# Performance work log

Hardware: AMD Instinct MI355X
Metric: run time of the kernel (lower is better)

Reference implementation:

```python
import jax, jax.numpy as jnp
import numpy as np

# Static dims (see shape_source)
B, S, D = 4, 4096, 1024      # batch, seq, d_model
H, E, K = 4096, 8, 2         # ffn hidden, num experts, top_k
GS = 128                     # group size = sqrt(B*S)
G = (B * S) // GS            # 128 groups, zero padding
CAP = 32                     # expert capacity after clamping


def setup_inputs() -> dict:
    key = jax.random.key(0)
    ks = jax.random.split(key, 8)
    std = jnp.float32(0.02)
    return {
        "x": jax.random.normal(ks[0], (B, S, D), jnp.float32),
        "gate_w": jax.random.normal(ks[1], (D, E), jnp.float32) * std,
        "gate_b": jnp.zeros((E,), jnp.float32),
        "keys": jax.random.normal(ks[2], (D, E, H), jnp.float32) * std,
        "key_b": jnp.zeros((E, H), jnp.float32),
        "values": jax.random.normal(ks[3], (H, E, D), jnp.float32) * std,
        "value_b": jnp.zeros((E, D), jnp.float32),
        "s_keys": jax.random.normal(ks[4], (D, 1, H), jnp.float32) * std,
        "s_key_b": jnp.zeros((1, H), jnp.float32),
        "s_values": jax.random.normal(ks[5], (H, 1, D), jnp.float32) * std,
        "s_value_b": jnp.zeros((1, D), jnp.float32),
    }


def reference(x, gate_w, gate_b, keys, key_b, values, value_b,
              s_keys, s_key_b, s_values, s_value_b):
    # ---- group tokens: [B,S,D] -> [G,GS,D] (B*S divisible by GS, no pad) ----
    xg = x.reshape(G, GS, D)

    # ---- Router (inference path: no aux loss) ----
    logits = jnp.einsum('gsd,de->gse', xg, gate_w) + gate_b          # [G,GS,E]
    probs = jax.nn.softmax(logits, axis=-1)
    gate, idx = jax.lax.top_k(probs, K)                              # [G,GS,K]
    mask = jax.nn.one_hot(idx, E, dtype=gate.dtype)                  # [G,GS,K,E]
    # position within each expert's capacity buffer (1-based where assigned)
    pos = jnp.cumsum(mask, axis=1) * mask                            # [G,GS,K,E]
    valid = (pos < CAP).astype(gate.dtype)
    pos_oh = jax.nn.one_hot(pos.astype(jnp.int32), CAP, dtype=gate.dtype)  # [G,GS,K,E,CAP]
    # combine tensor: sum over top-k, drop slot 0 (unassigned) -> [G,GS,E,CAP-1]
    combine = jnp.einsum('gsk,gske,gskec->gsec', gate, valid, pos_oh)[..., 1:]
    dispatch = (combine > 0).astype(x.dtype)                         # dispatch mask

    # ---- dispatch -> per-expert FFN -> combine ----
    exp_in = jnp.einsum('gsec,gsd->gecd', dispatch, xg)              # [G,E,CAP-1,D]
    h = jax.nn.gelu(jnp.einsum('gecd,deh->gech', exp_in, keys)
                    + key_b[None, :, None, :])                       # [G,E,CAP-1,H]
    eo = jnp.einsum('gech,hed->gecd', h, values) + value_b[None, :, None, :]
    moe = jnp.einsum('gsec,gecd->gsd', combine, eo)                  # [G,GS,D]

    # ---- shared expert (num_shared_experts == 1; mean over 1 is identity) ----
    sh = jax.nn.gelu(jnp.einsum('gsd,dh->gsh', xg, s_keys[:, 0, :]) + s_key_b[0])
    shared = jnp.einsum('gsh,hd->gsd', sh, s_values[:, 0, :]) + s_value_b[0]

    return (moe + shared).reshape(B, S, D)
```

## Files before the change

### kernel.cpp

```cpp
#include <hip/hip_runtime.h>
#include <hip/hip_bf16.h>

typedef unsigned short u16;
typedef __attribute__((ext_vector_type(8))) __bf16 bf16x8;
typedef __attribute__((ext_vector_type(4))) float f32x4;

#define TOK 16384
#define DM  1024
#define HD  4096
#define NE  8
#define NG  128
#define GSZ 128
#define CAPM 31
#define MEP (NG*32)

static __device__ __forceinline__ u16 f2b(float f) {
  union { float f; unsigned u; } v; v.f = f;
  unsigned r = v.u + 0x7fffu + ((v.u >> 16) & 1u);
  return (u16)(r >> 16);
}
static __device__ __forceinline__ float b2f(u16 u) {
  union { unsigned u; float f; } v; v.u = (unsigned)u << 16; return v.f;
}

static __device__ __forceinline__ float gelu_f(float x) {
  float y = 0.7978845608028654f * (x + 0.044715f * x * x * x);
  float t = __expf(-2.0f * fabsf(y));
  float th = (1.0f - t) / (1.0f + t);
  th = (y < 0.0f) ? -th : th;
  return 0.5f * x * (1.0f + th);
}

static __device__ __forceinline__ void gl2lds16(const void* g, void* l) {
  __builtin_amdgcn_global_load_lds(
      (const __attribute__((address_space(1))) void*)g,
      (__attribute__((address_space(3))) void*)l, 16, 0, 0);
}

__global__ __launch_bounds__(256) void k_router(
    const float* __restrict__ x, const float* __restrict__ gw,
    const float* __restrict__ gb, int* __restrict__ e_sel,
    float* __restrict__ gsel) {
  int wave = threadIdx.x >> 6, lane = threadIdx.x & 63;
  int t = blockIdx.x * 4 + wave;
  const float* xr = x + (size_t)t * DM;
  double acc[8] = {0,0,0,0,0,0,0,0};
  for (int d0 = lane * 4; d0 < DM; d0 += 256) {
    float4 xv = *(const float4*)(xr + d0);
    float xa[4] = {xv.x, xv.y, xv.z, xv.w};
    const float* g0 = gw + (size_t)d0 * NE;
#pragma unroll
    for (int dd = 0; dd < 4; ++dd)
#pragma unroll
      for (int e = 0; e < 8; ++e)
        acc[e] += (double)xa[dd] * (double)g0[dd * 8 + e];
  }
#pragma unroll
  for (int off = 32; off > 0; off >>= 1)
#pragma unroll
    for (int e = 0; e < 8; ++e)
      acc[e] += __shfl_down(acc[e], off, 64);
  if (lane == 0) {
    float l[8];
#pragma unroll
    for (int e = 0; e < 8; ++e) l[e] = (float)acc[e] + gb[e];
    int e0 = 0;
    for (int e = 1; e < 8; ++e) if (l[e] > l[e0]) e0 = e;
    int e1 = (e0 == 0) ? 1 : 0;
    for (int e = 0; e < 8; ++e) if (e != e0 && l[e] > l[e1]) e1 = e;
    float m = l[e0], s = 0.f, p[8];
    for (int e = 0; e < 8; ++e) { p[e] = expf(l[e] - m); s += p[e]; }
    e_sel[t] = e0; e_sel[TOK + t] = e1;
    gsel[t] = p[e0] / s; gsel[TOK + t] = p[e1] / s;
  }
}

__global__ void k_assign(const int* __restrict__ e_sel,
                         int* __restrict__ tok_slot, int* __restrict__ slot_tok) {
  int g = blockIdx.x;
  for (int i = threadIdx.x; i < NE * 32 * 2; i += 64) {
    int e = i >> 6, rem = i & 63, c = rem >> 1, k = rem & 1;
    slot_tok[((size_t)(e * MEP + g * 32 + c)) * 2 + k] = -1;
  }
  __syncthreads();
  if (threadIdx.x == 0) {
    int cnt[2][NE];
    for (int k = 0; k < 2; ++k) for (int e = 0; e < NE; ++e) cnt[k][e] = 0;
    for (int s = 0; s < GSZ; ++s) {
      int t = g * GSZ + s;
      for (int k = 0; k < 2; ++k) {
        int e = e_sel[k * TOK + t];
        int r = ++cnt[k][e];
        if (r <= CAPM) {
          int m = e * MEP + g * 32 + (r - 1);
          tok_slot[k * TOK + t] = m;
          slot_tok[(size_t)m * 2 + k] = t;
        } else tok_slot[k * TOK + t] = -1;
      }
    }
  }
}

__global__ __launch_bounds__(128) void k_build_expin(
    const float* __restrict__ x, const int* __restrict__ slot_tok,
    u16* __restrict__ exp_in) {
  int m = blockIdx.x;
  int t0 = slot_tok[(size_t)m * 2], t1 = slot_tok[(size_t)m * 2 + 1];
  int d = threadIdx.x * 8;
  float v[8] = {0,0,0,0,0,0,0,0};
  if (t0 >= 0) {
    const float4* p = (const float4*)(x + (size_t)t0 * DM + d);
    float4 a = p[0], b = p[1];
    v[0]+=a.x; v[1]+=a.y; v[2]+=a.z; v[3]+=a.w;
    v[4]+=b.x; v[5]+=b.y; v[6]+=b.z; v[7]+=b.w;
  }
  if (t1 >= 0) {
    const float4* p = (const float4*)(x + (size_t)t1 * DM + d);
    float4 a = p[0], b = p[1];
    v[0]+=a.x; v[1]+=a.y; v[2]+=a.z; v[3]+=a.w;
    v[4]+=b.x; v[5]+=b.y; v[6]+=b.z; v[7]+=b.w;
  }
  ushort4 o0, o1;
  o0.x=f2b(v[0]); o0.y=f2b(v[1]); o0.z=f2b(v[2]); o0.w=f2b(v[3]);
  o1.x=f2b(v[4]); o1.y=f2b(v[5]); o1.z=f2b(v[6]); o1.w=f2b(v[7]);
  *(ushort4*)(exp_in + (size_t)m * DM + d) = o0;
  *(ushort4*)(exp_in + (size_t)m * DM + d + 4) = o1;
}

__global__ __launch_bounds__(256) void k_cast_bf16(
    const float* __restrict__ in, u16* __restrict__ out, size_t n) {
  size_t i = ((size_t)blockIdx.x * 256 + threadIdx.x) * 4;
  if (i >= n) return;
  float4 v = *(const float4*)(in + i);
  ushort4 o; o.x=f2b(v.x); o.y=f2b(v.y); o.z=f2b(v.z); o.w=f2b(v.w);
  *(ushort4*)(out + i) = o;
}

__global__ __launch_bounds__(256) void k_transpose(
    const float* __restrict__ in, u16* __restrict__ out,
    int K, int N, int rs) {
  __shared__ float tile[32][33];
  int k0 = blockIdx.x * 32, n0 = blockIdx.y * 32;
  int tx = threadIdx.x & 31, ty = threadIdx.x >> 5;
#pragma unroll
  for (int i = 0; i < 4; ++i)
    tile[ty + i * 8][tx] = in[(size_t)(k0 + ty + i * 8) * rs + n0 + tx];
  __syncthreads();
#pragma unroll
  for (int i = 0; i < 4; ++i) {
    int n = ty + i * 8;
    out[(size_t)(n0 + n) * K + k0 + tx] = f2b(tile[tx][n]);
  }
}


#define PH_MID() \
  __builtin_amdgcn_s_barrier(); \
  __builtin_amdgcn_s_setprio(1);

#define PH_END() \
  __builtin_amdgcn_s_setprio(0); \
  asm volatile("s_waitcnt vmcnt(4)" ::: "memory"); \
  __builtin_amdgcn_s_barrier();

#define PH_END0() \
  __builtin_amdgcn_s_setprio(0); \
  asm volatile("s_waitcnt vmcnt(0)" ::: "memory"); \
  __builtin_amdgcn_s_barrier();

#define PH_ENDN() \
  __builtin_amdgcn_s_setprio(0); \
  __builtin_amdgcn_s_barrier();

#define STG(gp, ld, lds) \
  gl2lds16((gp) + (size_t)srow * (ld) + scol, (lds) + sdst); \
  gl2lds16((gp) + (size_t)(srow + 64) * (ld) + scol, (lds) + 4096 + sdst);

#define RD_A(SLOT) \
  _Pragma("unroll") for (int k2 = 0; k2 < 2; ++k2) \
    _Pragma("unroll") for (int mi = 0; mi < 4; ++mi) \
      a[k2][mi] = *(const bf16x8*)(&HA[SLOT][0] + offA[k2][mi]);

#define RD_BA(SLOT) \
  _Pragma("unroll") for (int k2 = 0; k2 < 2; ++k2) \
    _Pragma("unroll") for (int ni = 0; ni < 2; ++ni) \
      bA[k2][ni] = *(const bf16x8*)(&HB[SLOT][0] + offB[k2][ni]);

#define RD_BB(SLOT) \
  _Pragma("unroll") for (int k2 = 0; k2 < 2; ++k2) \
    _Pragma("unroll") for (int ni = 0; ni < 2; ++ni) \
      bB[k2][ni] = *(const bf16x8*)(&HB[SLOT][0] + offB[k2][ni]);

#define MM(BM, MOFF, NOFF) \
  _Pragma("unroll") for (int k2 = 0; k2 < 2; ++k2) \
    _Pragma("unroll") for (int mi = 0; mi < 4; ++mi) \
      _Pragma("unroll") for (int ni = 0; ni < 2; ++ni) \
        acc[mi + MOFF][ni + NOFF] = __builtin_amdgcn_mfma_f32_16x16x32_bf16( \
            a[k2][mi], BM[k2][ni], acc[mi + MOFF][ni + NOFF], 0, 0, 0);

#define TILE(T, SA0, SA1, SB0, SB1, DA0, DA1, DB0, DB1) { \
  const u16* An = Ab + ((T) + 1) * 64; \
  const u16* Bn = Bb + ((T) + 1) * 64; \
  RD_A(SA0); RD_BA(SB0); \
  STG(An, lda, &HA[DA0][0]); \
  PH_MID(); MM(bA, 0, 0); PH_END(); \
  RD_BB(SB1); \
  STG(Bn, ldb, &HB[DB0][0]); \
  PH_MID(); MM(bB, 0, 2); PH_END(); \
  RD_A(SA1); \
  STG(Bn + (size_t)128 * ldb, ldb, &HB[DB1][0]); \
  PH_MID(); MM(bB, 4, 2); PH_END(); \
  STG(An + (size_t)128 * lda, lda, &HA[DA1][0]); \
  PH_MID(); MM(bA, 4, 0); PH_END(); \
}

#define TILE_LAST(SA0, SA1, SB0, SB1) { \
  RD_A(SA0); RD_BA(SB0); \
  PH_MID(); MM(bA, 0, 0); PH_END0(); \
  RD_BB(SB1); \
  PH_MID(); MM(bB, 0, 2); PH_ENDN(); \
  RD_A(SA1); \
  PH_MID(); MM(bB, 4, 2); PH_ENDN(); \
  PH_MID(); MM(bA, 4, 0); PH_ENDN(); \
}

template <int EPI>
__global__ __launch_bounds__(512, 2) void k_gemm8p(
    const u16* __restrict__ A, size_t sAe, int lda,
    const u16* __restrict__ B, size_t sBe, int ldb,
    void* __restrict__ Cv, size_t sCe, int ldc,
    const float* __restrict__ bias, int sBiasE, int K, int gx, int gy) {
  __shared__ __align__(16) u16 HA[4][128 * 64];
  __shared__ __align__(16) u16 HB[4][128 * 64];
  const int tid = threadIdx.x;
  const int lane = tid & 63, wid = tid >> 6;
  const int wr = wid >> 2, wc = wid & 3;
  const int la15 = lane & 15, hi = lane >> 4;

  int nwg = gridDim.x, per = nwg >> 3;
  int wg = (blockIdx.x & 7) * per + (blockIdx.x >> 3);
  int bx = wg % gx, tmp = wg / gx;
  int by = tmp % gy, z = tmp / gy;

  const u16* Ab = A + (size_t)z * sAe + (size_t)(bx * 256) * lda;
  const u16* Bb = B + (size_t)z * sBe + (size_t)(by * 256) * ldb;

  int offA[2][4], offB[2][2];
#pragma unroll
  for (int k2 = 0; k2 < 2; ++k2) {
    int sl = k2 * 4 + hi;
#pragma unroll
    for (int mi = 0; mi < 4; ++mi) {
      int r = (mi * 2 + wr) * 16 + la15;
      offA[k2][mi] = r * 64 + ((sl ^ (r & 7)) << 3);
    }
#pragma unroll
    for (int ni = 0; ni < 2; ++ni) {
      int r = (ni * 4 + wc) * 16 + la15;
      offB[k2][ni] = r * 64 + ((sl ^ (r & 7)) << 3);
    }
  }
  const int srow = tid >> 3;
  const int scol = (((tid & 7) ^ (srow & 7)) << 3);
  const int sdst = (tid & ~63) * 8;

  f32x4 acc[8][4] = {};
  const int NT = K >> 6;

  bf16x8 a[2][4], bA[2][2], bB[2][2];

  STG(Ab, lda, &HA[0][0]);
  STG(Bb, ldb, &HB[0][0]);
  STG(Bb + (size_t)128 * ldb, ldb, &HB[1][0]);
  STG(Ab + (size_t)128 * lda, lda, &HA[1][0]);
  asm volatile("s_waitcnt vmcnt(0)" ::: "memory");
  __builtin_amdgcn_s_barrier();

  for (int t = 0; t + 2 < NT; t += 2) {
    TILE(t,     0, 1, 0, 1, 2, 3, 2, 3);
    TILE(t + 1, 2, 3, 2, 3, 0, 1, 0, 1);
  }
  TILE(NT - 2, 0, 1, 0, 1, 2, 3, 2, 3);
  TILE_LAST(2, 3, 2, 3);

  const int hi4 = hi << 2;
#pragma unroll
  for (int ni = 0; ni < 4; ++ni) {
    int col = by * 256 + (ni * 4 + wc) * 16 + la15;
    float bv = bias[(size_t)z * sBiasE + col];
#pragma unroll
    for (int mi = 0; mi < 8; ++mi) {
      int row0 = bx * 256 + (mi * 2 + wr) * 16 + hi4;
      f32x4 v = acc[mi][ni];
#pragma unroll
      for (int j = 0; j < 4; ++j) {
        int row = row0 + j;
        float val = v[j] + bv;
        if (EPI == 0)
          ((u16*)Cv)[(size_t)z * sCe + (size_t)row * ldc + col] = f2b(gelu_f(val));
        else if (EPI == 1)
          ((u16*)Cv)[(size_t)z * sCe + (size_t)row * ldc + col] = f2b(val);
        else
          ((float*)Cv)[(size_t)z * sCe + (size_t)row * ldc + col] = val;
      }
    }
  }
}

__global__ __launch_bounds__(256) void k_combine(
    const int* __restrict__ tok_slot, const float* __restrict__ gsel,
    const u16* __restrict__ eo, float* __restrict__ out) {
  int t = blockIdx.x;
  int d = threadIdx.x * 4;
  float4 v = *(float4*)(out + (size_t)t * DM + d);
#pragma unroll
  for (int k = 0; k < 2; ++k) {
    int m = tok_slot[k * TOK + t];
    if (m >= 0) {
      float g = gsel[k * TOK + t];
      ushort4 e = *(const ushort4*)(eo + (size_t)m * DM + d);
      v.x += g * b2f(e.x); v.y += g * b2f(e.y);
      v.z += g * b2f(e.z); v.w += g * b2f(e.w);
    }
  }
  *(float4*)(out + (size_t)t * DM + d) = v;
}

__global__ void k_report(float* out, float code) { out[0] = code; }

extern "C" void kernel_launch(void* const* d_in, const int* in_sizes, int n_in,
                              void* d_out, int out_size, void* d_ws, size_t ws_size,
                              hipStream_t stream) {
  (void)in_sizes; (void)n_in;
  const float* x     = (const float*)d_in[0];
  const float* gw    = (const float*)d_in[1];
  const float* gb    = (const float*)d_in[2];
  const float* keys  = (const float*)d_in[3];
  const float* keyb  = (const float*)d_in[4];
  const float* vals  = (const float*)d_in[5];
  const float* valb  = (const float*)d_in[6];
  const float* skey  = (const float*)d_in[7];
  const float* skeyb = (const float*)d_in[8];
  const float* sval  = (const float*)d_in[9];
  const float* svalb = (const float*)d_in[10];
  float* out = (float*)d_out;

  char* ws = (char*)d_ws;
  size_t off = 0;
  auto alloc = [&](size_t bytes) -> char* {
    char* p = ws + off; off += (bytes + 255) & ~(size_t)255; return p;
  };
  int*   e_sel    = (int*)  alloc(2 * TOK * 4);
  float* gsel     = (float*)alloc(2 * TOK * 4);
  int*   tok_slot = (int*)  alloc(2 * TOK * 4);
  int*   slot_tok = (int*)  alloc((size_t)NE * MEP * 2 * 4);

  size_t off_r1 = off;
  u16* xb     = (u16*)alloc((size_t)TOK * DM * 2);
  u16* skT    = (u16*)alloc((size_t)HD * DM * 2);
  u16* svT    = (u16*)alloc((size_t)DM * HD * 2);
  u16* exp_in = (u16*)alloc((size_t)NE * MEP * DM * 2);
  u16* eo = (u16*)(ws + off_r1);
  size_t eo_end = off_r1 + (size_t)NE * MEP * DM * 2;
  if (eo_end > off) off = eo_end;

  u16* keysT = (u16*)alloc((size_t)NE * HD * DM * 2);
  u16* valsT = (u16*)alloc((size_t)NE * DM * HD * 2);

  size_t sh_b = (size_t)TOK * HD * 2;
  size_t h_b  = (size_t)NE * MEP * HD * 2;
  u16* sh = (u16*)(ws + off);
  u16* h  = (u16*)(ws + off);
  size_t need = off + (sh_b > h_b ? sh_b : h_b);

  if (need > ws_size) {
    hipMemsetAsync(d_out, 0, (size_t)out_size * 4, stream);
    k_report<<<1, 1, 0, stream>>>(out, -(float)(ws_size >> 20));
    return;
  }

  k_router<<<TOK / 4, 256, 0, stream>>>(x, gw, gb, e_sel, gsel);
  k_assign<<<NG, 64, 0, stream>>>(e_sel, tok_slot, slot_tok);
  k_build_expin<<<NE * MEP, 128, 0, stream>>>(x, slot_tok, exp_in);

  k_cast_bf16<<<(TOK * DM / 4) / 256, 256, 0, stream>>>(x, xb, (size_t)TOK * DM);
  k_transpose<<<dim3(DM / 32, HD / 32), 256, 0, stream>>>(skey, skT, DM, HD, HD);
  k_transpose<<<dim3(HD / 32, DM / 32), 256, 0, stream>>>(sval, svT, HD, DM, DM);
  for (int e = 0; e < NE; ++e) {
    k_transpose<<<dim3(DM / 32, HD / 32), 256, 0, stream>>>(
        keys + (size_t)e * HD, keysT + (size_t)e * HD * DM, DM, HD, NE * HD);
    k_transpose<<<dim3(HD / 32, DM / 32), 256, 0, stream>>>(
        vals + (size_t)e * DM, valsT + (size_t)e * DM * HD, HD, DM, NE * DM);
  }

  k_gemm8p<0><<<(TOK/256)*(HD/256), 512, 0, stream>>>(
      xb, 0, DM, skT, 0, DM, sh, 0, HD, skeyb, 0, DM, TOK/256, HD/256);
  k_gemm8p<2><<<(TOK/256)*(DM/256), 512, 0, stream>>>(
      sh, 0, HD, svT, 0, HD, out, 0, DM, svalb, 0, HD, TOK/256, DM/256);

  k_gemm8p<0><<<(MEP/256)*(HD/256)*NE, 512, 0, stream>>>(
      exp_in, (size_t)MEP * DM, DM, keysT, (size_t)HD * DM, DM,
      h, (size_t)MEP * HD, HD, keyb, HD, DM, MEP/256, HD/256);
  k_gemm8p<1><<<(MEP/256)*(DM/256)*NE, 512, 0, stream>>>(
      h, (size_t)MEP * HD, HD, valsT, (size_t)DM * HD, HD,
      eo, (size_t)MEP * DM, DM, valb, DM, HD, MEP/256, DM/256);

  k_combine<<<TOK, 256, 0, stream>>>(tok_slot, gsel, eo, out);
}
```

Before: 1.244 ms.

## Software-pipeline LDS fragment reads with double-buffered A registers in GEMM

Restructures the GEMM main loop so that LDS fragment reads for the next phase are issued before the current phase's MFMAs. It adds a second A register buffer (aC/aN) and prefetches the next tile's A and B fragments at the end of each tile. The barriers drop from two per phase to one, with looser vmcnt waits, and the per-lane LDS offsets are simplified to base plus constant strides. The aim is to hide LDS latency behind MFMA work and cut synchronisation cost, at the price of higher register pressure under launch_bounds(512,2) and tighter reasoning about LDS hazards.

```diff
diff --git a/kernel.cpp b/kernel.cpp
--- a/kernel.cpp
+++ b/kernel.cpp
@@ -154,74 +154,62 @@
 }
 
 
-#define PH_MID() \
-  __builtin_amdgcn_s_barrier(); \
-  __builtin_amdgcn_s_setprio(1);
-
-#define PH_END() \
-  __builtin_amdgcn_s_setprio(0); \
-  asm volatile("s_waitcnt vmcnt(4)" ::: "memory"); \
-  __builtin_amdgcn_s_barrier();
-
-#define PH_END0() \
-  __builtin_amdgcn_s_setprio(0); \
-  asm volatile("s_waitcnt vmcnt(0)" ::: "memory"); \
-  __builtin_amdgcn_s_barrier();
-
-#define PH_ENDN() \
-  __builtin_amdgcn_s_setprio(0); \
-  __builtin_amdgcn_s_barrier();
+#define SP1() __builtin_amdgcn_s_setprio(1);
+#define SP0() __builtin_amdgcn_s_setprio(0);
+#define BAR() __builtin_amdgcn_s_barrier();
+#define VM2() asm volatile("s_waitcnt vmcnt(2)" ::: "memory");
+#define VM0() asm volatile("s_waitcnt vmcnt(0)" ::: "memory");
 
 #define STG(gp, ld, lds) \
   gl2lds16((gp) + (size_t)srow * (ld) + scol, (lds) + sdst); \
   gl2lds16((gp) + (size_t)(srow + 64) * (ld) + scol, (lds) + 4096 + sdst);
 
-#define RD_A(SLOT) \
+#define RD_A(DST, SLOT) \
   _Pragma("unroll") for (int k2 = 0; k2 < 2; ++k2) \
     _Pragma("unroll") for (int mi = 0; mi < 4; ++mi) \
-      a[k2][mi] = *(const bf16x8*)(&HA[SLOT][0] + offA[k2][mi]);
-
-#define RD_BA(SLOT) \
+      DST[k2][mi] = *(const bf16x8*)(&HA[SLOT][0] + offAk[k2] + mi * 2048);
+
+#define RD_B(DST, SLOT) \
   _Pragma("unroll") for (int k2 = 0; k2 < 2; ++k2) \
     _Pragma("unroll") for (int ni = 0; ni < 2; ++ni) \
-      bA[k2][ni] = *(const bf16x8*)(&HB[SLOT][0] + offB[k2][ni]);
-
-#define RD_BB(SLOT) \
-  _Pragma("unroll") for (int k2 = 0; k2 < 2; ++k2) \
-    _Pragma("unroll") for (int ni = 0; ni < 2; ++ni) \
-      bB[k2][ni] = *(const bf16x8*)(&HB[SLOT][0] + offB[k2][ni]);
-
-#define MM(BM, MOFF, NOFF) \
+      DST[k2][ni] = *(const bf16x8*)(&HB[SLOT][0] + offBk[k2] + ni * 4096);
+
+#define MMA(AM, BM, MOFF, NOFF) \
   _Pragma("unroll") for (int k2 = 0; k2 < 2; ++k2) \
     _Pragma("unroll") for (int mi = 0; mi < 4; ++mi) \
       _Pragma("unroll") for (int ni = 0; ni < 2; ++ni) \
         acc[mi + MOFF][ni + NOFF] = __builtin_amdgcn_mfma_f32_16x16x32_bf16( \
-            a[k2][mi], BM[k2][ni], acc[mi + MOFF][ni + NOFF], 0, 0, 0);
+            AM[k2][mi], BM[k2][ni], acc[mi + MOFF][ni + NOFF], 0, 0, 0);
 
 #define TILE(T, SA0, SA1, SB0, SB1, DA0, DA1, DB0, DB1) { \
   const u16* An = Ab + ((T) + 1) * 64; \
   const u16* Bn = Bb + ((T) + 1) * 64; \
-  RD_A(SA0); RD_BA(SB0); \
-  STG(An, lda, &HA[DA0][0]); \
-  PH_MID(); MM(bA, 0, 0); PH_END(); \
-  RD_BB(SB1); \
-  STG(Bn, ldb, &HB[DB0][0]); \
-  PH_MID(); MM(bB, 0, 2); PH_END(); \
-  RD_A(SA1); \
+   \
+  RD_B(bB, SB1); STG(An, lda, &HA[DA0][0]); \
+  SP1(); MMA(aC, bA, 0, 0); SP0(); \
+  VM2(); BAR(); \
+   \
+  RD_A(aN, SA1); STG(Bn, ldb, &HB[DB0][0]); \
+  SP1(); MMA(aC, bB, 0, 2); SP0(); \
+  BAR(); \
+   \
   STG(Bn + (size_t)128 * ldb, ldb, &HB[DB1][0]); \
-  PH_MID(); MM(bB, 4, 2); PH_END(); \
-  STG(An + (size_t)128 * lda, lda, &HA[DA1][0]); \
-  PH_MID(); MM(bA, 4, 0); PH_END(); \
+  SP1(); MMA(aN, bB, 4, 2); SP0(); \
+  VM2(); BAR(); \
+   \
+  RD_A(aC, DA0); STG(An + (size_t)128 * lda, lda, &HA[DA1][0]); \
+  SP1(); MMA(aN, bA, 4, 0); SP0(); \
+  RD_B(bA, DB0); \
+  VM2(); BAR(); \
 }
 
 #define TILE_LAST(SA0, SA1, SB0, SB1) { \
-  RD_A(SA0); RD_BA(SB0); \
-  PH_MID(); MM(bA, 0, 0); PH_END0(); \
-  RD_BB(SB1); \
-  PH_MID(); MM(bB, 0, 2); PH_ENDN(); \
-  RD_A(SA1); \
-  PH_MID(); MM(bB, 4, 2); PH_ENDN(); \
-  PH_MID(); MM(bA, 4, 0); PH_ENDN(); \
+  RD_B(bB, SB1); \
+  SP1(); MMA(aC, bA, 0, 0); SP0(); \
+  VM0(); BAR(); \
+  RD_A(aN, SA1); \
+  SP1(); MMA(aC, bB, 0, 2); \
+  MMA(aN, bB, 4, 2); MMA(aN, bA, 4, 0); SP0(); \
 }
 
 template <int EPI>
@@ -245,20 +233,12 @@
   const u16* Ab = A + (size_t)z * sAe + (size_t)(bx * 256) * lda;
   const u16* Bb = B + (size_t)z * sBe + (size_t)(by * 256) * ldb;
 
-  int offA[2][4], offB[2][2];
+  int offAk[2], offBk[2];
 #pragma unroll
   for (int k2 = 0; k2 < 2; ++k2) {
-    int sl = k2 * 4 + hi;
-#pragma unroll
-    for (int mi = 0; mi < 4; ++mi) {
-      int r = (mi * 2 + wr) * 16 + la15;
-      offA[k2][mi] = r * 64 + ((sl ^ (r & 7)) << 3);
-    }
-#pragma unroll
-    for (int ni = 0; ni < 2; ++ni) {
-      int r = (ni * 4 + wc) * 16 + la15;
-      offB[k2][ni] = r * 64 + ((sl ^ (r & 7)) << 3);
-    }
+    int sw = (((k2 * 4 + hi) ^ (la15 & 7)) << 3);
+    offAk[k2] = (wr * 16 + la15) * 64 + sw;
+    offBk[k2] = (wc * 16 + la15) * 64 + sw;
   }
   const int srow = tid >> 3;
   const int scol = (((tid & 7) ^ (srow & 7)) << 3);
@@ -267,14 +247,14 @@
   f32x4 acc[8][4] = {};
   const int NT = K >> 6;
 
-  bf16x8 a[2][4], bA[2][2], bB[2][2];
+  bf16x8 aC[2][4], aN[2][4], bA[2][2], bB[2][2];
 
   STG(Ab, lda, &HA[0][0]);
   STG(Bb, ldb, &HB[0][0]);
   STG(Bb + (size_t)128 * ldb, ldb, &HB[1][0]);
   STG(Ab + (size_t)128 * lda, lda, &HA[1][0]);
-  asm volatile("s_waitcnt vmcnt(0)" ::: "memory");
-  __builtin_amdgcn_s_barrier();
+  VM2(); BAR();
+  RD_A(aC, 0); RD_B(bA, 0);
 
   for (int t = 0; t + 2 < NT; t += 2) {
     TILE(t,     0, 1, 0, 1, 2, 3, 2, 3);
```

Result: slower. 1.910 ms (+53.5%).
